# Kernel optimization log

Measured on AMD Instinct MI355X. Metric: run time of the kernel, lower is better.

Reference implementation:

```python
import jax, jax.numpy as jnp
import numpy as np

CAPACITY_FRAC = 0.5


def setup_inputs() -> dict:
    key = jax.random.key(0)
    ks = jax.random.split(key, 5)
    B, T, D, F = 4, 8192, 1024, 4096
    x = jax.random.normal(ks[0], (B, T, D), dtype=jnp.float32)
    w_router = jax.random.normal(ks[1], (D,), dtype=jnp.float32) / np.sqrt(D)
    w1 = jax.random.normal(ks[2], (D, F), dtype=jnp.float32) / np.sqrt(D)
    b1 = jnp.zeros((F,), dtype=jnp.float32)
    w2 = jax.random.normal(ks[3], (F, D), dtype=jnp.float32) / np.sqrt(F)
    b2 = jnp.zeros((D,), dtype=jnp.float32)
    return {"x": x, "w_router": w_router, "w1": w1, "b1": b1, "w2": w2, "b2": b2}


def _ffn_block(h, w1, b1, w2, b2):
    # standard transformer FFN wrapped by MixtureOfDepths
    return jax.nn.gelu(h @ w1 + b1) @ w2 + b2


def reference(x, w_router, w1, b1, w2, b2):
    B, T, D = x.shape
    capacity = max(1, int(T * CAPACITY_FRAC))
    # router: Linear(d_model, 1, bias=False) -> scores [B, T]
    scores = x @ w_router
    # top-k token selection per sequence
    _, tok_idx = jax.lax.top_k(scores, capacity)  # [B, capacity]
    # gather selected tokens: [B, capacity, D]
    selected = jnp.take_along_axis(x, tok_idx[:, :, None], axis=1)
    processed = _ffn_block(selected, w1, b1, w2, b2)
    # scatter processed tokens back into a copy of x (topk indices are unique per row)
    b_idx = jnp.arange(B)[:, None]
    out = x.at[b_idx, tok_idx].set(processed)
    return out
```

## Files before the change

### kernel.cpp

```cpp
#include <hip/hip_runtime.h>
#include <stdint.h>

typedef float v4f __attribute__((ext_vector_type(4)));
typedef short v8s __attribute__((ext_vector_type(8)));

constexpr int Bq = 4, Tq = 8192, Dq = 1024, Fq = 4096;
constexpr int CAP = Tq / 2;
constexpr int Mq  = Bq * CAP;

__device__ __forceinline__ unsigned short f2bf(float f) {
  unsigned int u = __float_as_uint(f);
  u += 0x7FFFu + ((u >> 16) & 1u);
  return (unsigned short)(u >> 16);
}

__device__ __forceinline__ void async_cp16(const void* g, void* l) {
  __builtin_amdgcn_global_load_lds(
      (__attribute__((address_space(1))) void*)g,
      (__attribute__((address_space(3))) void*)l, 16, 0, 0);
}

__global__ void scores_kernel(const float* __restrict__ x,
                              const float* __restrict__ wr_g,
                              double* __restrict__ scores) {
  __shared__ __align__(16) float wr[Dq];
  for (int i = threadIdx.x; i < Dq; i += 256) wr[i] = wr_g[i];
  __syncthreads();
  int wid = threadIdx.x >> 6, lane = threadIdx.x & 63;
  int gw = blockIdx.x * 4 + wid;
  const float4* wp = (const float4*)wr;
  for (int rr = 0; rr < 4; ++rr) {
    int row = gw * 4 + rr;
    const float4* xp = (const float4*)(x + (size_t)row * Dq);
    double s = 0.0;
#pragma unroll
    for (int q = 0; q < 4; ++q) {
      float4 v = xp[lane + q * 64];
      float4 w = wp[lane + q * 64];
      s += (double)v.x * w.x + (double)v.y * w.y + (double)v.z * w.z + (double)v.w * w.w;
    }
#pragma unroll
    for (int off = 32; off; off >>= 1) s += __shfl_down(s, off);
    if (lane == 0) scores[row] = s;
  }
}

__device__ __forceinline__ int block_reduce_i(int v, int* red, int tid) {
#pragma unroll
  for (int off = 32; off; off >>= 1) v += __shfl_down(v, off);
  __syncthreads();
  if ((tid & 63) == 0) red[tid >> 6] = v;
  __syncthreads();
  int s = 0;
#pragma unroll
  for (int k = 0; k < 16; ++k) s += red[k];
  return s;
}

__global__ __launch_bounds__(1024) void select_topk(const double* __restrict__ scores,
                                                    int* __restrict__ selIdx,
                                                    unsigned char* __restrict__ selFlag) {
  int b = blockIdx.x, tid = threadIdx.x;
  const double* s = scores + (size_t)b * Tq;
  __shared__ int red[16];
  __shared__ int counter;
  unsigned long long key[8];
#pragma unroll
  for (int i = 0; i < 8; ++i) {
    unsigned long long u = (unsigned long long)__double_as_longlong(s[tid + i * 1024]);
    key[i] = (u >> 63) ? ~u : (u | 0x8000000000000000ULL);
  }
  unsigned long long cutoff = 0ULL;
  for (int bit = 63; bit >= 0; --bit) {
    unsigned long long cand = cutoff | (1ULL << bit);
    int c = 0;
#pragma unroll
    for (int i = 0; i < 8; ++i) c += (key[i] >= cand) ? 1 : 0;
    int tot = block_reduce_i(c, red, tid);
    if (tot >= CAP) cutoff = cand;
  }
  int cGt = 0, cEq = 0;
#pragma unroll
  for (int i = 0; i < 8; ++i) { cGt += (key[i] > cutoff); cEq += (key[i] == cutoff); }
  int gtTot = block_reduce_i(cGt, red, tid);
  int eqTot = block_reduce_i(cEq, red, tid);
  int need = CAP - gtTot;
  if (tid == 0) counter = 0;
  __syncthreads();
  bool takeAllEq = (eqTot == need);
#pragma unroll
  for (int i = 0; i < 8; ++i) {
    int t = tid + i * 1024;
    bool sel = takeAllEq ? (key[i] >= cutoff) : (key[i] > cutoff);
    if (sel) { int pos = atomicAdd(&counter, 1); selIdx[b * CAP + pos] = t; }
    selFlag[(size_t)b * Tq + t] = sel ? (unsigned char)1 : (unsigned char)0;
  }
  if (!takeAllEq) {
    __syncthreads();
    if (tid == 0) {
      int taken = 0;
      for (int t = 0; t < Tq && taken < need; ++t) {
        unsigned long long u = (unsigned long long)__double_as_longlong(s[t]);
        unsigned long long k = (u >> 63) ? ~u : (u | 0x8000000000000000ULL);
        if (k == cutoff) {
          selIdx[b * CAP + gtTot + taken] = t;
          selFlag[(size_t)b * Tq + t] = 1;
          ++taken;
        }
      }
    }
  }
}

__global__ void gather_kernel(const float* __restrict__ x,
                              const int* __restrict__ selIdx,
                              unsigned short* __restrict__ Xs) {
  int wid = threadIdx.x >> 6, lane = threadIdx.x & 63;
  int m = blockIdx.x * 4 + wid;
  int b = m >> 12;
  int tok = selIdx[m];
  const float4* src = (const float4*)(x + ((size_t)b * Tq + tok) * Dq);
  ushort4* dst = (ushort4*)(Xs + (size_t)m * Dq);
#pragma unroll
  for (int q = 0; q < 4; ++q) {
    float4 v = src[lane + q * 64];
    ushort4 o; o.x = f2bf(v.x); o.y = f2bf(v.y); o.z = f2bf(v.z); o.w = f2bf(v.w);
    dst[lane + q * 64] = o;
  }
}

__global__ void copy_pass(const float* __restrict__ x,
                          const unsigned char* __restrict__ selFlag,
                          float* __restrict__ out) {
  int wid = threadIdx.x >> 6, lane = threadIdx.x & 63;
  int row = blockIdx.x * 4 + wid;
  if (selFlag[row]) return;
  const float4* src = (const float4*)(x + (size_t)row * Dq);
  float4* dst = (float4*)(out + (size_t)row * Dq);
#pragma unroll
  for (int q = 0; q < 4; ++q) dst[lane + q * 64] = src[lane + q * 64];
}

__global__ void transpose_f32_to_bf16(const float* __restrict__ in,
                                      unsigned short* __restrict__ out,
                                      int R, int C) {
  __shared__ float tile[32][33];
  int tx = threadIdx.x, ty = threadIdx.y;
  int c0 = blockIdx.x * 32, r0 = blockIdx.y * 32;
#pragma unroll
  for (int k = 0; k < 4; ++k)
    tile[ty + k * 8][tx] = in[(size_t)(r0 + ty + k * 8) * C + c0 + tx];
  __syncthreads();
#pragma unroll
  for (int k = 0; k < 4; ++k)
    out[(size_t)(c0 + ty + k * 8) * R + r0 + tx] = f2bf(tile[tx][ty + k * 8]);
}

__global__ __launch_bounds__(256) void gemm1_gelu(const unsigned short* __restrict__ A,
                                                  const unsigned short* __restrict__ Bt,
                                                  const float* __restrict__ bias,
                                                  unsigned short* __restrict__ H) {
  constexpr int K = Dq, N = Fq;
  __shared__ __align__(16) unsigned short As[128 * 32];
  __shared__ __align__(16) unsigned short Bs[128 * 32];
  const int tid = threadIdx.x;
  const int wid = tid >> 6, lane = tid & 63;
  const int wm = wid >> 1, wn = wid & 1;
  const int quad = lane >> 4, l16 = lane & 15;
  const int m0 = blockIdx.y * 128, n0 = blockIdx.x * 128;

  const int sRow = tid >> 2, sCol = (tid & 3) << 3;
  const unsigned short* aG0 = A + (size_t)(m0 + sRow) * K + sCol;
  const unsigned short* aG1 = aG0 + (size_t)64 * K;
  const unsigned short* bG0 = Bt + (size_t)(n0 + sRow) * K + sCol;
  const unsigned short* bG1 = bG0 + (size_t)64 * K;
  unsigned short* aL0 = As + wid * 512;
  unsigned short* aL1 = As + 2048 + wid * 512;
  unsigned short* bL0 = Bs + wid * 512;
  unsigned short* bL1 = Bs + 2048 + wid * 512;

  int aOff[4], bOff[4];
#pragma unroll
  for (int i = 0; i < 4; ++i) aOff[i] = (wm * 64 + i * 16 + l16) * 32 + quad * 8;
#pragma unroll
  for (int j = 0; j < 4; ++j) bOff[j] = (wn * 64 + j * 16 + l16) * 32 + quad * 8;

  v4f acc[4][4] = {};

  for (int k0 = 0; k0 < K; k0 += 32) {
    async_cp16(aG0 + k0, aL0);
    async_cp16(aG1 + k0, aL1);
    async_cp16(bG0 + k0, bL0);
    async_cp16(bG1 + k0, bL1);
    __syncthreads();
    v8s af[4], bfr[4];
#pragma unroll
    for (int i = 0; i < 4; ++i) af[i] = *(const v8s*)(As + aOff[i]);
#pragma unroll
    for (int j = 0; j < 4; ++j) bfr[j] = *(const v8s*)(Bs + bOff[j]);
#pragma unroll
    for (int i = 0; i < 4; ++i)
#pragma unroll
      for (int j = 0; j < 4; ++j)
        acc[i][j] = __builtin_amdgcn_mfma_f32_16x16x32_bf16(af[i], bfr[j], acc[i][j], 0, 0, 0);
    __syncthreads();
  }

  const int mBase = m0 + wm * 64, nBase = n0 + wn * 64;
#pragma unroll
  for (int i = 0; i < 4; ++i)
#pragma unroll
    for (int r = 0; r < 4; ++r) {
      const int row = mBase + i * 16 + quad * 4 + r;
      unsigned short* hp = H + (size_t)row * N;
#pragma unroll
      for (int j = 0; j < 4; ++j) {
        const int col = nBase + j * 16 + l16;
        float c = acc[i][j][r] + bias[col];
        float z = 0.7978845608028654f * (c + 0.044715f * c * c * c);
        float a = __expf(-2.0f * fabsf(z));
        float th = copysignf((1.0f - a) / (1.0f + a), z);
        hp[col] = f2bf(0.5f * c * (1.0f + th));
      }
    }
}

__global__ __launch_bounds__(256) void gemm2_scatter(const unsigned short* __restrict__ A,
                                                     const unsigned short* __restrict__ Bt,
                                                     const float* __restrict__ bias,
                                                     const int* __restrict__ selIdx,
                                                     float* __restrict__ out,
                                                     int chunkStart) {
  constexpr int K = Fq, N = Dq;
  __shared__ __align__(16) unsigned short As[128 * 32];
  __shared__ __align__(16) unsigned short Bs[128 * 32];
  const int tid = threadIdx.x;
  const int wid = tid >> 6, lane = tid & 63;
  const int wm = wid >> 1, wn = wid & 1;
  const int quad = lane >> 4, l16 = lane & 15;
  const int m0 = blockIdx.y * 128, n0 = blockIdx.x * 128;

  const int sRow = tid >> 2, sCol = (tid & 3) << 3;
  const unsigned short* aG0 = A + (size_t)(m0 + sRow) * K + sCol;
  const unsigned short* aG1 = aG0 + (size_t)64 * K;
  const unsigned short* bG0 = Bt + (size_t)(n0 + sRow) * K + sCol;
  const unsigned short* bG1 = bG0 + (size_t)64 * K;
  unsigned short* aL0 = As + wid * 512;
  unsigned short* aL1 = As + 2048 + wid * 512;
  unsigned short* bL0 = Bs + wid * 512;
  unsigned short* bL1 = Bs + 2048 + wid * 512;

  int aOff[4], bOff[4];
#pragma unroll
  for (int i = 0; i < 4; ++i) aOff[i] = (wm * 64 + i * 16 + l16) * 32 + quad * 8;
#pragma unroll
  for (int j = 0; j < 4; ++j) bOff[j] = (wn * 64 + j * 16 + l16) * 32 + quad * 8;

  v4f acc[4][4] = {};

  for (int k0 = 0; k0 < K; k0 += 32) {
    async_cp16(aG0 + k0, aL0);
    async_cp16(aG1 + k0, aL1);
    async_cp16(bG0 + k0, bL0);
    async_cp16(bG1 + k0, bL1);
    __syncthreads();
    v8s af[4], bfr[4];
#pragma unroll
    for (int i = 0; i < 4; ++i) af[i] = *(const v8s*)(As + aOff[i]);
#pragma unroll
    for (int j = 0; j < 4; ++j) bfr[j] = *(const v8s*)(Bs + bOff[j]);
#pragma unroll
    for (int i = 0; i < 4; ++i)
#pragma unroll
      for (int j = 0; j < 4; ++j)
        acc[i][j] = __builtin_amdgcn_mfma_f32_16x16x32_bf16(af[i], bfr[j], acc[i][j], 0, 0, 0);
    __syncthreads();
  }

  const int mBase = m0 + wm * 64, nBase = n0 + wn * 64;
#pragma unroll
  for (int i = 0; i < 4; ++i)
#pragma unroll
    for (int r = 0; r < 4; ++r) {
      const int lrow = mBase + i * 16 + quad * 4 + r;
      const int m = chunkStart + lrow;
      const int b = m >> 12;
      const int tok = selIdx[m];
      float* op = out + ((size_t)b * Tq + tok) * Dq;
#pragma unroll
      for (int j = 0; j < 4; ++j) {
        const int col = nBase + j * 16 + l16;
        op[col] = acc[i][j][r] + bias[col];
      }
    }
}

extern "C" void kernel_launch(void* const* d_in, const int* in_sizes, int n_in,
                              void* d_out, int out_size, void* d_ws, size_t ws_size,
                              hipStream_t stream) {
  const float* x        = (const float*)d_in[0];
  const float* w_router = (const float*)d_in[1];
  const float* w1       = (const float*)d_in[2];
  const float* b1       = (const float*)d_in[3];
  const float* w2       = (const float*)d_in[4];
  const float* b2       = (const float*)d_in[5];
  float* out = (float*)d_out;

  char* p = (char*)d_ws;
  auto alloc = [&](size_t bytes) {
    char* r = p;
    p += (bytes + 255) & ~(size_t)255;
    return r;
  };
  double* scores          = (double*)alloc((size_t)Bq * Tq * 8);
  int* selIdx             = (int*)alloc((size_t)Mq * 4);
  unsigned char* selFlag  = (unsigned char*)alloc((size_t)Bq * Tq);
  unsigned short* W1t     = (unsigned short*)alloc((size_t)Dq * Fq * 2);
  unsigned short* W2t     = (unsigned short*)alloc((size_t)Dq * Fq * 2);
  unsigned short* Xs      = (unsigned short*)alloc((size_t)Mq * Dq * 2);
  size_t used = (size_t)(p - (char*)d_ws);
  size_t rem = ws_size > used ? ws_size - used : 0;
  int chunkRows = (int)(rem / ((size_t)Fq * 2));
  chunkRows = (chunkRows / 128) * 128;
  if (chunkRows > Mq) chunkRows = Mq;
  if (chunkRows < 128) chunkRows = 128;
  unsigned short* H = (unsigned short*)p;

  transpose_f32_to_bf16<<<dim3(Fq / 32, Dq / 32), dim3(32, 8), 0, stream>>>(w1, W1t, Dq, Fq);
  transpose_f32_to_bf16<<<dim3(Dq / 32, Fq / 32), dim3(32, 8), 0, stream>>>(w2, W2t, Fq, Dq);
  scores_kernel<<<2048, 256, 0, stream>>>(x, w_router, scores);
  select_topk<<<Bq, 1024, 0, stream>>>(scores, selIdx, selFlag);
  gather_kernel<<<Mq / 4, 256, 0, stream>>>(x, selIdx, Xs);
  copy_pass<<<(Bq * Tq) / 4, 256, 0, stream>>>(x, selFlag, out);

  for (int r0 = 0; r0 < Mq; r0 += chunkRows) {
    int rows = (Mq - r0 < chunkRows) ? (Mq - r0) : chunkRows;
    gemm1_gelu<<<dim3(Fq / 128, rows / 128), 256, 0, stream>>>(
        Xs + (size_t)r0 * Dq, W1t, b1, H);
    gemm2_scatter<<<dim3(Dq / 128, rows / 128), 256, 0, stream>>>(
        H, W2t, b2, selIdx, out, r0);
  }
}
```

Baseline: 765.3 us.

## Swizzle LDS layout, group block order for L2 reuse, streamline GELU epilogue

Both GEMM kernels now use an XOR swizzle on the 16-byte column slot in LDS, applied identically to the async global-to-LDS copies and the fragment reads, to cut LDS bank conflicts. The 2D grid becomes a 1D grid remapped so that groups of 8 M-panels share each N-panel, which should improve L2 reuse of the weight tiles. The epilogues hoist the bias loads into registers, and GELU now uses an fma polynomial, exp2f and a hardware reciprocal. The reciprocal slightly lowers precision, and the grouped block order relies on the panel count being divisible by 8, falling back to row-major order otherwise.

```diff
diff --git a/kernel.cpp b/kernel.cpp
--- a/kernel.cpp
+++ b/kernel.cpp
@@ -156,10 +156,12 @@
     out[(size_t)(c0 + ty + k * 8) * R + r0 + tx] = f2bf(tile[tx][ty + k * 8]);
 }
 
+
 __global__ __launch_bounds__(256) void gemm1_gelu(const unsigned short* __restrict__ A,
                                                   const unsigned short* __restrict__ Bt,
                                                   const float* __restrict__ bias,
-                                                  unsigned short* __restrict__ H) {
+                                                  unsigned short* __restrict__ H,
+                                                  int nPanels) {
   constexpr int K = Dq, N = Fq;
   __shared__ __align__(16) unsigned short As[128 * 32];
   __shared__ __align__(16) unsigned short Bs[128 * 32];
@@ -167,9 +169,20 @@
   const int wid = tid >> 6, lane = tid & 63;
   const int wm = wid >> 1, wn = wid & 1;
   const int quad = lane >> 4, l16 = lane & 15;
-  const int m0 = blockIdx.y * 128, n0 = blockIdx.x * 128;
-
-  const int sRow = tid >> 2, sCol = (tid & 3) << 3;
+
+  int l = blockIdx.x;
+  int pIdx, nIdx;
+  if ((nPanels & 7) == 0) {
+    nIdx = (l >> 3) & 31;
+    pIdx = (l & 7) | ((l >> 8) << 3);
+  } else {
+    nIdx = l & 31;
+    pIdx = l >> 5;
+  }
+  const int m0 = pIdx * 128, n0 = nIdx * 128;
+
+  const int sRow = tid >> 2;
+  const int sCol = (((tid & 3) ^ ((sRow >> 1) & 3)) << 3);
   const unsigned short* aG0 = A + (size_t)(m0 + sRow) * K + sCol;
   const unsigned short* aG1 = aG0 + (size_t)64 * K;
   const unsigned short* bG0 = Bt + (size_t)(n0 + sRow) * K + sCol;
@@ -179,11 +192,12 @@
   unsigned short* bL0 = Bs + wid * 512;
   unsigned short* bL1 = Bs + 2048 + wid * 512;
 
+  const int swz = ((quad ^ ((l16 >> 1) & 3)) << 3);
   int aOff[4], bOff[4];
 #pragma unroll
-  for (int i = 0; i < 4; ++i) aOff[i] = (wm * 64 + i * 16 + l16) * 32 + quad * 8;
-#pragma unroll
-  for (int j = 0; j < 4; ++j) bOff[j] = (wn * 64 + j * 16 + l16) * 32 + quad * 8;
+  for (int i = 0; i < 4; ++i) aOff[i] = (wm * 64 + i * 16 + l16) * 32 + swz;
+#pragma unroll
+  for (int j = 0; j < 4; ++j) bOff[j] = (wn * 64 + j * 16 + l16) * 32 + swz;
 
   v4f acc[4][4] = {};
 
@@ -207,6 +221,11 @@
   }
 
   const int mBase = m0 + wm * 64, nBase = n0 + wn * 64;
+  float bv[4];
+#pragma unroll
+  for (int j = 0; j < 4; ++j) bv[j] = bias[nBase + j * 16 + l16];
+  const float kA = 0.7978845608028654f, kB = 0.044715f * 0.7978845608028654f;
+  const float kE = -2.0f * 1.4426950408889634f;
 #pragma unroll
   for (int i = 0; i < 4; ++i)
 #pragma unroll
@@ -216,10 +235,10 @@
 #pragma unroll
       for (int j = 0; j < 4; ++j) {
         const int col = nBase + j * 16 + l16;
-        float c = acc[i][j][r] + bias[col];
-        float z = 0.7978845608028654f * (c + 0.044715f * c * c * c);
-        float a = __expf(-2.0f * fabsf(z));
-        float th = copysignf((1.0f - a) / (1.0f + a), z);
+        float c = acc[i][j][r] + bv[j];
+        float z = c * __builtin_fmaf(kB, c * c, kA);
+        float a = exp2f(kE * fabsf(z));
+        float th = copysignf((1.0f - a) * __builtin_amdgcn_rcpf(1.0f + a), z);
         hp[col] = f2bf(0.5f * c * (1.0f + th));
       }
     }
@@ -230,7 +249,7 @@
                                                      const float* __restrict__ bias,
                                                      const int* __restrict__ selIdx,
                                                      float* __restrict__ out,
-                                                     int chunkStart) {
+                                                     int chunkStart, int nPanels) {
   constexpr int K = Fq, N = Dq;
   __shared__ __align__(16) unsigned short As[128 * 32];
   __shared__ __align__(16) unsigned short Bs[128 * 32];
@@ -238,9 +257,20 @@
   const int wid = tid >> 6, lane = tid & 63;
   const int wm = wid >> 1, wn = wid & 1;
   const int quad = lane >> 4, l16 = lane & 15;
-  const int m0 = blockIdx.y * 128, n0 = blockIdx.x * 128;
-
-  const int sRow = tid >> 2, sCol = (tid & 3) << 3;
+
+  int l = blockIdx.x;
+  int pIdx, nIdx;
+  if ((nPanels & 7) == 0) {
+    nIdx = (l >> 3) & 7;
+    pIdx = (l & 7) | ((l >> 6) << 3);
+  } else {
+    nIdx = l & 7;
+    pIdx = l >> 3;
+  }
+  const int m0 = pIdx * 128, n0 = nIdx * 128;
+
+  const int sRow = tid >> 2;
+  const int sCol = (((tid & 3) ^ ((sRow >> 1) & 3)) << 3);
   const unsigned short* aG0 = A + (size_t)(m0 + sRow) * K + sCol;
   const unsigned short* aG1 = aG0 + (size_t)64 * K;
   const unsigned short* bG0 = Bt + (size_t)(n0 + sRow) * K + sCol;
@@ -250,11 +280,12 @@
   unsigned short* bL0 = Bs + wid * 512;
   unsigned short* bL1 = Bs + 2048 + wid * 512;
 
+  const int swz = ((quad ^ ((l16 >> 1) & 3)) << 3);
   int aOff[4], bOff[4];
 #pragma unroll
-  for (int i = 0; i < 4; ++i) aOff[i] = (wm * 64 + i * 16 + l16) * 32 + quad * 8;
-#pragma unroll
-  for (int j = 0; j < 4; ++j) bOff[j] = (wn * 64 + j * 16 + l16) * 32 + quad * 8;
+  for (int i = 0; i < 4; ++i) aOff[i] = (wm * 64 + i * 16 + l16) * 32 + swz;
+#pragma unroll
+  for (int j = 0; j < 4; ++j) bOff[j] = (wn * 64 + j * 16 + l16) * 32 + swz;
 
   v4f acc[4][4] = {};
 
@@ -278,6 +309,9 @@
   }
 
   const int mBase = m0 + wm * 64, nBase = n0 + wn * 64;
+  float bv[4];
+#pragma unroll
+  for (int j = 0; j < 4; ++j) bv[j] = bias[nBase + j * 16 + l16];
 #pragma unroll
   for (int i = 0; i < 4; ++i)
 #pragma unroll
@@ -290,7 +324,7 @@
 #pragma unroll
       for (int j = 0; j < 4; ++j) {
         const int col = nBase + j * 16 + l16;
-        op[col] = acc[i][j][r] + bias[col];
+        op[col] = acc[i][j][r] + bv[j];
       }
     }
 }
@@ -335,9 +369,8 @@
 
   for (int r0 = 0; r0 < Mq; r0 += chunkRows) {
     int rows = (Mq - r0 < chunkRows) ? (Mq - r0) : chunkRows;
-    gemm1_gelu<<<dim3(Fq / 128, rows / 128), 256, 0, stream>>>(
-        Xs + (size_t)r0 * Dq, W1t, b1, H);
-    gemm2_scatter<<<dim3(Dq / 128, rows / 128), 256, 0, stream>>>(
-        H, W2t, b2, selIdx, out, r0);
-  }
-}
+    int p1 = rows / 128;
+    gemm1_gelu<<<32 * p1, 256, 0, stream>>>(Xs + (size_t)r0 * Dq, W1t, b1, H, p1);
+    gemm2_scatter<<<8 * p1, 256, 0, stream>>>(H, W2t, b2, selIdx, out, r0, p1);
+  }
+}
```

After: 698.9 us. 1.1x faster.
